# Kernel tuning notes

Measured on AMD Instinct MI355X. Metric: run time of the kernel, lower is better.

The kernel has to match this reference:

```python
import jax, jax.numpy as jnp
import numpy as np

RES_LIST = (16, 23, 32, 46, 64, 92, 128, 184, 256, 368, 512, 736)
NUM_DIM = 3
N_FEATURES = 2
LOG2_HASHMAP = 19
MAX_PARAMS = 2 ** LOG2_HASHMAP
N_POINTS = 2_000_000
PRIMES = (1, 2654435761, 805459861)  # Instant-NGP spatial hash primes


def _grid_meta():
    offsets, off = [], 0
    for r in RES_LIST:
        p = min(MAX_PARAMS, r ** NUM_DIM)
        p = int(np.ceil(p / 8) * 8)  # align to 8 as in __init__
        offsets.append(off)
        off += p
    offsets.append(off)
    return np.array(offsets, np.int32), off


def setup_inputs() -> dict:
    key = jax.random.key(0)
    k1, k2 = jax.random.split(key)
    offsets_np, total = _grid_meta()
    inputs = jax.random.uniform(k1, (N_POINTS, NUM_DIM), dtype=jnp.float32)
    std = 1e-4  # reset_parameters(): uniform(-1e-4, 1e-4)
    embeddings = jax.random.uniform(k2, (total, N_FEATURES), dtype=jnp.float32,
                                    minval=-std, maxval=std)
    return {
        "inputs": inputs,
        "embeddings": embeddings,
        "offsets_list": jnp.asarray(offsets_np),
        "resolutions_list": jnp.asarray(np.array(RES_LIST, np.int32)),
    }


def _encode(inputs, embeddings, offsets_list, resolutions_list):
    N = inputs.shape[0]
    F = embeddings.shape[1]
    params_in_level = (offsets_list[1:] - offsets_list[:-1]).astype(jnp.uint32)
    res = resolutions_list.astype(jnp.int32)
    # hash only when the dense grid does not fit in the hashmap
    use_hash = (res * res * res) > MAX_PARAMS  # res^3 < 2^31, safe in int32
    p0 = jnp.uint32(PRIMES[0]); p1 = jnp.uint32(PRIMES[1]); p2 = jnp.uint32(PRIMES[2])

    def level_fn(r, off, pil, uh):
        scale = (r - 1).astype(inputs.dtype)
        pos = inputs * scale                      # [N,3] in [0, res-1)
        f0 = jnp.floor(pos)
        w = pos - f0                              # trilinear fractions
        f0u = f0.astype(jnp.uint32)
        ru = r.astype(jnp.uint32)
        out = jnp.zeros((N, F), embeddings.dtype)
        for c in range(2 ** NUM_DIM):             # 8 corners (fixed small loop)
            bits = jnp.array([(c >> d) & 1 for d in range(NUM_DIM)], jnp.uint32)
            idx = f0u + bits                      # [N,3] corner grid coords
            wb = jnp.where(bits.astype(bool), w, 1.0 - w)
            weight = wb[:, 0] * wb[:, 1] * wb[:, 2]
            lin = idx[:, 0] + idx[:, 1] * ru + idx[:, 2] * ru * ru
            h = (idx[:, 0] * p0) ^ (idx[:, 1] * p1) ^ (idx[:, 2] * p2)
            flat = jnp.where(uh, h, lin) % pil    # uint32 wraparound hash
            g = embeddings[off + flat.astype(jnp.int32)]  # [N,F] gather
            out = out + weight[:, None] * g
        return out

    outs = jax.vmap(level_fn)(res, offsets_list[:-1], params_in_level, use_hash)
    # [L,N,F] -> [N, L*F], matching permute(1,0,2).reshape
    return outs.transpose(1, 0, 2).reshape(N, -1)


def reference(inputs, embeddings, offsets_list, resolutions_list):
    return _encode(inputs, embeddings, offsets_list, resolutions_list)
```

## Files before the change

kernel.cpp:

```cpp
#include <hip/hip_runtime.h>
#include <hip/hip_fp16.h>


namespace {
constexpr int NLEV = 12;
constexpr int BLOCK = 256;
constexpr int TOTAL = 4078528;
constexpr int DENSE_A_END = 146368;
constexpr int L4_SIZE = 262144;
constexpr unsigned P1 = 2654435761u;
constexpr unsigned P2 = 805459861u;
constexpr unsigned HMASK = (1u << 19) - 1u;

__device__ __constant__ constexpr int kRes[NLEV] = {
    16, 23, 32, 46, 64, 92, 128, 184, 256, 368, 512, 736};
__device__ __constant__ constexpr int kOff[NLEV] = {
    0, 4096, 16264, 49032, 146368, 408512,
    932800, 1457088, 1981376, 2505664, 3029952, 3554240};

typedef float    f32x2 __attribute__((ext_vector_type(2)));
typedef unsigned u32x2 __attribute__((ext_vector_type(2)));

__device__ __forceinline__ unsigned pkh2(float a, float b) {
    __half2 h = __floats2half2_rn(a, b);
    return *reinterpret_cast<unsigned*>(&h);
}
__device__ __forceinline__ float lo2f(unsigned u) {
    __half2 h = *reinterpret_cast<__half2*>(&u);
    return __low2float(h);
}
__device__ __forceinline__ float hi2f(unsigned u) {
    __half2 h = *reinterpret_cast<__half2*>(&u);
    return __high2float(h);
}
}

__global__ void __launch_bounds__(BLOCK)
pack_table_kernel(const float2* __restrict__ emb,
                  unsigned* __restrict__ packed, int total)
{
    int i = blockIdx.x * BLOCK + threadIdx.x;
    if (i < total) {
        float2 v = emb[i];
        packed[i] = pkh2(v.x, v.y);
    }
}

__global__ void __launch_bounds__(BLOCK)
pack_quad_kernel(const float2* __restrict__ emb, uint4* __restrict__ quad)
{
    int i = blockIdx.x * BLOCK + threadIdx.x;
    if (i >= DENSE_A_END) return;
    int R = (i < 4096) ? 16 : (i < 16264) ? 23 : (i < 49032) ? 32 : 46;
    float2 e0 = emb[i];
    float2 e1 = emb[i + 1];
    float2 e2 = emb[i + R];
    float2 e3 = emb[i + R + 1];
    uint4 q;
    q.x = pkh2(e0.x, e0.y); q.y = pkh2(e1.x, e1.y);
    q.z = pkh2(e2.x, e2.y); q.w = pkh2(e3.x, e3.y);
    quad[i] = q;
}

__global__ void __launch_bounds__(BLOCK)
pack_pair4_kernel(const float2* __restrict__ emb, u32x2* __restrict__ pair4)
{
    int i = blockIdx.x * BLOCK + threadIdx.x;
    if (i >= L4_SIZE) return;
    int g = DENSE_A_END + i;
    float2 a = emb[g];
    float2 b = emb[g + 1];
    u32x2 o;
    o.x = pkh2(a.x, a.y);
    o.y = pkh2(b.x, b.y);
    pair4[i] = o;
}

__global__ void __launch_bounds__(BLOCK)
dense_a_kernel(const float* __restrict__ inp, const uint4* __restrict__ quad,
               unsigned* __restrict__ stage, int N)
{
    const int tid = blockIdx.x * BLOCK + threadIdx.x;
    const int p0 = 2 * tid;
    if (p0 >= N) return;

    const f32x2* ip2 = reinterpret_cast<const f32x2*>(inp);
    const f32x2 v0 = ip2[3 * tid + 0];
    const f32x2 v1 = ip2[3 * tid + 1];
    const f32x2 v2 = ip2[3 * tid + 2];
    const float X[2] = {v0.x, v1.y};
    const float Y[2] = {v0.y, v2.x};
    const float Z[2] = {v1.x, v2.y};

#pragma unroll
    for (int l = 0; l < 4; ++l) {
        const unsigned R = (unsigned)kRes[l];
        const unsigned R2 = R * R;
        const float scale = (float)(kRes[l] - 1);
        const uint4* qt = quad + kOff[l];
        u32x2 res;
#pragma unroll
        for (int k = 0; k < 2; ++k) {
            const float px = X[k] * scale, py = Y[k] * scale, pz = Z[k] * scale;
            const float fx = floorf(px), fy = floorf(py), fz = floorf(pz);
            const float rx = px - fx, ry = py - fy, rz = pz - fz;
            const unsigned ix = (unsigned)fx, iy = (unsigned)fy,
                           iz = (unsigned)fz;
            const unsigned base = ix + iy * R + iz * R2;
            const uint4 q0 = qt[base];
            const uint4 q1 = qt[base + R2];
            const float wx0 = 1.0f - rx, wx1 = rx;
            const float wy0 = 1.0f - ry, wy1 = ry;
            const float wz0 = 1.0f - rz, wz1 = rz;
            const float ex00 = wx0 * lo2f(q0.x) + wx1 * lo2f(q0.y);
            const float ey00 = wx0 * hi2f(q0.x) + wx1 * hi2f(q0.y);
            const float ex10 = wx0 * lo2f(q0.z) + wx1 * lo2f(q0.w);
            const float ey10 = wx0 * hi2f(q0.z) + wx1 * hi2f(q0.w);
            const float ex01 = wx0 * lo2f(q1.x) + wx1 * lo2f(q1.y);
            const float ey01 = wx0 * hi2f(q1.x) + wx1 * hi2f(q1.y);
            const float ex11 = wx0 * lo2f(q1.z) + wx1 * lo2f(q1.w);
            const float ey11 = wx0 * hi2f(q1.z) + wx1 * hi2f(q1.w);
            const float sx = wz0 * (wy0 * ex00 + wy1 * ex10) +
                             wz1 * (wy0 * ex01 + wy1 * ex11);
            const float sy = wz0 * (wy0 * ey00 + wy1 * ey10) +
                             wz1 * (wy0 * ey01 + wy1 * ey11);
            res[k] = pkh2(sx, sy);
        }
        if (p0 + 1 < N) {
            __builtin_nontemporal_store(
                res, reinterpret_cast<u32x2*>(&stage[(long long)l * N + p0]));
        } else {
            __builtin_nontemporal_store(res.x, &stage[(long long)l * N + p0]);
        }
    }
}

__global__ void __launch_bounds__(BLOCK)
dense_b_kernel(const float* __restrict__ inp, const u32x2* __restrict__ pair4,
               unsigned* __restrict__ stage4, int N)
{
    const int tid = blockIdx.x * BLOCK + threadIdx.x;
    const int p0 = 2 * tid;
    if (p0 >= N) return;

    const f32x2* ip2 = reinterpret_cast<const f32x2*>(inp);
    const f32x2 v0 = ip2[3 * tid + 0];
    const f32x2 v1 = ip2[3 * tid + 1];
    const f32x2 v2 = ip2[3 * tid + 2];
    const float X[2] = {v0.x, v1.y};
    const float Y[2] = {v0.y, v2.x};
    const float Z[2] = {v1.x, v2.y};

    constexpr unsigned R = 64, R2 = 4096;
    constexpr float scale = 63.0f;
    u32x2 res;
#pragma unroll
    for (int k = 0; k < 2; ++k) {
        const float px = X[k] * scale, py = Y[k] * scale, pz = Z[k] * scale;
        const float fx = floorf(px), fy = floorf(py), fz = floorf(pz);
        const float rx = px - fx, ry = py - fy, rz = pz - fz;
        const unsigned ix = (unsigned)fx, iy = (unsigned)fy, iz = (unsigned)fz;
        const unsigned base = ix + iy * R + iz * R2;
        const u32x2 q00 = pair4[base];
        const u32x2 q10 = pair4[base + R];
        const u32x2 q01 = pair4[base + R2];
        const u32x2 q11 = pair4[base + R2 + R];
        const float wx0 = 1.0f - rx, wx1 = rx;
        const float wy0 = 1.0f - ry, wy1 = ry;
        const float wz0 = 1.0f - rz, wz1 = rz;
        const float w00 = wy0 * wz0, w10 = wy1 * wz0;
        const float w01 = wy0 * wz1, w11 = wy1 * wz1;
        float sx = 0.0f, sy = 0.0f;
        sx = fmaf(w00 * wx0, lo2f(q00.x), fmaf(w00 * wx1, lo2f(q00.y), sx));
        sy = fmaf(w00 * wx0, hi2f(q00.x), fmaf(w00 * wx1, hi2f(q00.y), sy));
        sx = fmaf(w10 * wx0, lo2f(q10.x), fmaf(w10 * wx1, lo2f(q10.y), sx));
        sy = fmaf(w10 * wx0, hi2f(q10.x), fmaf(w10 * wx1, hi2f(q10.y), sy));
        sx = fmaf(w01 * wx0, lo2f(q01.x), fmaf(w01 * wx1, lo2f(q01.y), sx));
        sy = fmaf(w01 * wx0, hi2f(q01.x), fmaf(w01 * wx1, hi2f(q01.y), sy));
        sx = fmaf(w11 * wx0, lo2f(q11.x), fmaf(w11 * wx1, lo2f(q11.y), sx));
        sy = fmaf(w11 * wx0, hi2f(q11.x), fmaf(w11 * wx1, hi2f(q11.y), sy));
        res[k] = pkh2(sx, sy);
    }
    if (p0 + 1 < N) {
        __builtin_nontemporal_store(res, reinterpret_cast<u32x2*>(&stage4[p0]));
    } else {
        __builtin_nontemporal_store(res.x, &stage4[p0]);
    }
}

template <int L>
__device__ __forceinline__ unsigned
encode_hash(float x, float y, float z, const unsigned* __restrict__ pt)
{
    const float scale = (float)(kRes[L] - 1);
    const float px = x * scale, py = y * scale, pz = z * scale;
    const float fx = floorf(px), fy = floorf(py), fz = floorf(pz);
    const float rx = px - fx, ry = py - fy, rz = pz - fz;
    const unsigned ix = (unsigned)fx, iy = (unsigned)fy, iz = (unsigned)fz;
    const unsigned yA = iy * P1, yB = yA + P1;
    const unsigned zA = iz * P2, zB = zA + P2;
    const unsigned h00 = (ix ^ yA ^ zA) & HMASK;
    const unsigned h10 = (ix ^ yB ^ zA) & HMASK;
    const unsigned h01 = (ix ^ yA ^ zB) & HMASK;
    const unsigned h11 = (ix ^ yB ^ zB) & HMASK;

    const u32x2* pt2 = reinterpret_cast<const u32x2*>(pt);
    const u32x2 q00 = pt2[h00 >> 1];
    const u32x2 q10 = pt2[h10 >> 1];
    const u32x2 q01 = pt2[h01 >> 1];
    const u32x2 q11 = pt2[h11 >> 1];

    unsigned e00 = (h00 & 1) ? q00.y : q00.x;
    unsigned e10 = (h10 & 1) ? q10.y : q10.x;
    unsigned e01 = (h01 & 1) ? q01.y : q01.x;
    unsigned e11 = (h11 & 1) ? q11.y : q11.x;
    unsigned f00 = (h00 & 1) ? q00.x : q00.y;
    unsigned f10 = (h10 & 1) ? q10.x : q10.y;
    unsigned f01 = (h01 & 1) ? q01.x : q01.y;
    unsigned f11 = (h11 & 1) ? q11.x : q11.y;

    if (ix & 1u) {
        const unsigned xo = ix + 1u;
        f00 = pt[(xo ^ yA ^ zA) & HMASK];
        f10 = pt[(xo ^ yB ^ zA) & HMASK];
        f01 = pt[(xo ^ yA ^ zB) & HMASK];
        f11 = pt[(xo ^ yB ^ zB) & HMASK];
    }

    const float wx0 = 1.0f - rx, wx1 = rx;
    const float wy0 = 1.0f - ry, wy1 = ry;
    const float wz0 = 1.0f - rz, wz1 = rz;
    const float w00 = wy0 * wz0, w10 = wy1 * wz0;
    const float w01 = wy0 * wz1, w11 = wy1 * wz1;
    float sx = 0.0f, sy = 0.0f;
    sx = fmaf(w00 * wx0, lo2f(e00), fmaf(w00 * wx1, lo2f(f00), sx));
    sy = fmaf(w00 * wx0, hi2f(e00), fmaf(w00 * wx1, hi2f(f00), sy));
    sx = fmaf(w10 * wx0, lo2f(e10), fmaf(w10 * wx1, lo2f(f10), sx));
    sy = fmaf(w10 * wx0, hi2f(e10), fmaf(w10 * wx1, hi2f(f10), sy));
    sx = fmaf(w01 * wx0, lo2f(e01), fmaf(w01 * wx1, lo2f(f01), sx));
    sy = fmaf(w01 * wx0, hi2f(e01), fmaf(w01 * wx1, hi2f(f01), sy));
    sx = fmaf(w11 * wx0, lo2f(e11), fmaf(w11 * wx1, lo2f(f11), sx));
    sy = fmaf(w11 * wx0, hi2f(e11), fmaf(w11 * wx1, hi2f(f11), sy));
    return pkh2(sx, sy);
}

template <int L>
__global__ void __launch_bounds__(BLOCK)
hash_kernel(const float* __restrict__ inp, const unsigned* __restrict__ packed,
            unsigned* __restrict__ stage_l, int N)
{
    const int tid = blockIdx.x * BLOCK + threadIdx.x;
    const int p0 = 2 * tid;
    if (p0 >= N) return;

    const f32x2* ip2 = reinterpret_cast<const f32x2*>(inp);
    const f32x2 v0 = ip2[3 * tid + 0];
    const f32x2 v1 = ip2[3 * tid + 1];
    const f32x2 v2 = ip2[3 * tid + 2];

    const unsigned* pt = packed + kOff[L];
    u32x2 res;
    res.x = encode_hash<L>(v0.x, v0.y, v1.x, pt);
    res.y = encode_hash<L>(v1.y, v2.x, v2.y, pt);

    if (p0 + 1 < N) {
        __builtin_nontemporal_store(res, reinterpret_cast<u32x2*>(&stage_l[p0]));
    } else {
        __builtin_nontemporal_store(res.x, &stage_l[p0]);
    }
}

__global__ void __launch_bounds__(BLOCK)
assemble_kernel(const unsigned* __restrict__ lvl, float* __restrict__ out,
                int N)
{
    __shared__ float s_out[BLOCK * 25];
    const int t = threadIdx.x;
    const int n = blockIdx.x * BLOCK + t;

    if (n < N) {
#pragma unroll
        for (int l = 0; l < NLEV; ++l) {
            unsigned u = __builtin_nontemporal_load(&lvl[(long long)l * N + n]);
            s_out[t * 25 + 2 * l + 0] = lo2f(u);
            s_out[t * 25 + 2 * l + 1] = hi2f(u);
        }
    }
    __syncthreads();

    const long long base = (long long)blockIdx.x * (BLOCK * 24);
    const long long lim = (long long)N * 24;
#pragma unroll
    for (int k = 0; k < 24; ++k) {
        const int g = k * BLOCK + t;
        const long long gg = base + g;
        if (gg < lim) {
            const int nl = g / 24;
            const int j = g - nl * 24;
            __builtin_nontemporal_store(s_out[nl * 25 + j], &out[gg]);
        }
    }
}

template <int PACKED>
__global__ void __launch_bounds__(BLOCK, 4)
fused_kernel(const float* __restrict__ inp, const void* __restrict__ table,
             float* __restrict__ out, int N)
{
    __shared__ float s_out[BLOCK * 25];
    const int t = threadIdx.x;
    const int n = blockIdx.x * BLOCK + t;

    if (n < N) {
        const float x = inp[n * 3 + 0];
        const float y = inp[n * 3 + 1];
        const float z = inp[n * 3 + 2];

#pragma unroll
        for (int l = 0; l < NLEV; ++l) {
            const int R = kRes[l];
            const bool HASH = (l >= 5);
            const float scale = (float)(R - 1);
            const float px = x * scale, py = y * scale, pz = z * scale;
            const float fx = floorf(px), fy = floorf(py), fz = floorf(pz);
            const float wx = px - fx, wy = py - fy, wz = pz - fz;
            const unsigned ix = (unsigned)fx, iy = (unsigned)fy,
                           iz = (unsigned)fz;
            unsigned x0, x1, y0, y1, z0, z1;
            if (HASH) {
                x0 = ix;      x1 = ix + 1u;
                y0 = iy * P1; y1 = y0 + P1;
                z0 = iz * P2; z1 = z0 + P2;
            } else {
                const unsigned Ru = (unsigned)R, R2 = Ru * Ru;
                x0 = ix;      x1 = ix + 1u;
                y0 = iy * Ru; y1 = y0 + Ru;
                z0 = iz * R2; z1 = z0 + R2;
            }
            unsigned idx[8];
            if (HASH) {
                idx[0] = (x0 ^ y0 ^ z0) & HMASK; idx[1] = (x1 ^ y0 ^ z0) & HMASK;
                idx[2] = (x0 ^ y1 ^ z0) & HMASK; idx[3] = (x1 ^ y1 ^ z0) & HMASK;
                idx[4] = (x0 ^ y0 ^ z1) & HMASK; idx[5] = (x1 ^ y0 ^ z1) & HMASK;
                idx[6] = (x0 ^ y1 ^ z1) & HMASK; idx[7] = (x1 ^ y1 ^ z1) & HMASK;
            } else {
                idx[0] = x0 + y0 + z0; idx[1] = x1 + y0 + z0;
                idx[2] = x0 + y1 + z0; idx[3] = x1 + y1 + z0;
                idx[4] = x0 + y0 + z1; idx[5] = x1 + y0 + z1;
                idx[6] = x0 + y1 + z1; idx[7] = x1 + y1 + z1;
            }
            float ex[8], ey[8];
            if (PACKED) {
                const unsigned* eb =
                    reinterpret_cast<const unsigned*>(table) + kOff[l];
#pragma unroll
                for (int c = 0; c < 8; ++c) {
                    unsigned uu = eb[idx[c]];
                    ex[c] = lo2f(uu); ey[c] = hi2f(uu);
                }
            } else {
                const float2* eb =
                    reinterpret_cast<const float2*>(table) + kOff[l];
#pragma unroll
                for (int c = 0; c < 8; ++c) {
                    float2 e = eb[idx[c]]; ex[c] = e.x; ey[c] = e.y;
                }
            }
            const float w0x = 1.0f - wx, w0y = 1.0f - wy, w0z = 1.0f - wz;
            const float w00 = w0x * w0y, w10 = wx * w0y;
            const float w01 = w0x * wy,  w11 = wx * wy;
            const float wt[8] = {w00 * w0z, w10 * w0z, w01 * w0z, w11 * w0z,
                                 w00 * wz,  w10 * wz,  w01 * wz,  w11 * wz};
            float sx = 0.0f, sy = 0.0f;
#pragma unroll
            for (int c = 0; c < 8; ++c) {
                sx = fmaf(wt[c], ex[c], sx);
                sy = fmaf(wt[c], ey[c], sy);
            }
            s_out[t * 25 + 2 * l + 0] = sx;
            s_out[t * 25 + 2 * l + 1] = sy;
        }
    }
    __syncthreads();
    const long long base = (long long)blockIdx.x * (BLOCK * 24);
    const long long lim = (long long)N * 24;
#pragma unroll
    for (int k = 0; k < 24; ++k) {
        const int g = k * BLOCK + t;
        const long long gg = base + g;
        if (gg < lim) {
            const int nl = g / 24;
            const int j = g - nl * 24;
            out[gg] = s_out[nl * 25 + j];
        }
    }
}

extern "C" void kernel_launch(void* const* d_in, const int* in_sizes, int n_in,
                              void* d_out, int out_size, void* d_ws, size_t ws_size,
                              hipStream_t stream) {
    const float* inputs = (const float*)d_in[0];
    const float* embeddings = (const float*)d_in[1];
    float* out = (float*)d_out;

    const int N = in_sizes[0] / 3;
    const int total = in_sizes[1] / 2;

    const size_t quad_bytes = (size_t)DENSE_A_END * 16;
    const size_t pair4_bytes = (size_t)L4_SIZE * 8;
    const size_t packed_bytes = (size_t)total * sizeof(unsigned);
    const size_t stage_bytes = (size_t)NLEV * N * sizeof(unsigned);

    const int ngrid = (N + BLOCK - 1) / BLOCK;
    const int grid2 = (N / 2 + BLOCK - 1) / BLOCK;

    if (ws_size >= quad_bytes + pair4_bytes + packed_bytes + stage_bytes) {
        char* w = (char*)d_ws;
        uint4* quad = (uint4*)w;                  w += quad_bytes;
        u32x2* pair4 = (u32x2*)w;                 w += pair4_bytes;
        unsigned* packed = (unsigned*)w;          w += packed_bytes;
        unsigned* stage = (unsigned*)w;

        pack_table_kernel<<<(total + BLOCK - 1) / BLOCK, BLOCK, 0, stream>>>(
            (const float2*)embeddings, packed, total);
        pack_quad_kernel<<<(DENSE_A_END + BLOCK - 1) / BLOCK, BLOCK, 0, stream>>>(
            (const float2*)embeddings, quad);
        pack_pair4_kernel<<<(L4_SIZE + BLOCK - 1) / BLOCK, BLOCK, 0, stream>>>(
            (const float2*)embeddings, pair4);

        dense_a_kernel<<<grid2, BLOCK, 0, stream>>>(inputs, quad, stage, N);
        dense_b_kernel<<<grid2, BLOCK, 0, stream>>>(inputs, pair4,
                                                    stage + 4LL * N, N);
        hash_kernel<5><<<grid2, BLOCK, 0, stream>>>(inputs, packed, stage + 5LL * N, N);
        hash_kernel<6><<<grid2, BLOCK, 0, stream>>>(inputs, packed, stage + 6LL * N, N);
        hash_kernel<7><<<grid2, BLOCK, 0, stream>>>(inputs, packed, stage + 7LL * N, N);
        hash_kernel<8><<<grid2, BLOCK, 0, stream>>>(inputs, packed, stage + 8LL * N, N);
        hash_kernel<9><<<grid2, BLOCK, 0, stream>>>(inputs, packed, stage + 9LL * N, N);
        hash_kernel<10><<<grid2, BLOCK, 0, stream>>>(inputs, packed, stage + 10LL * N, N);
        hash_kernel<11><<<grid2, BLOCK, 0, stream>>>(inputs, packed, stage + 11LL * N, N);
        assemble_kernel<<<ngrid, BLOCK, 0, stream>>>(stage, out, N);
    } else if (ws_size >= packed_bytes) {
        unsigned* packed = (unsigned*)d_ws;
        pack_table_kernel<<<(total + BLOCK - 1) / BLOCK, BLOCK, 0, stream>>>(
            (const float2*)embeddings, packed, total);
        fused_kernel<1><<<ngrid, BLOCK, 0, stream>>>(inputs, packed, out, N);
    } else {
        fused_kernel<0><<<ngrid, BLOCK, 0, stream>>>(inputs, embeddings, out, N);
    }
}
```

Measured before the change: 530.2 us.

## Merge pack kernels and fuse per-level encode kernels into one launch

Combines the three embedding-packing kernels into one pack kernel that reads each embedding once for the flat table and reuses it for the quad and pair layouts. Replaces the nine per-level encode launches (dense A, dense B, seven hash levels) with one kernel whose block index selects the level group, so all levels can run concurrently across the GPU. This targets launch overhead and the tail idle time between small dependent launches. In exchange the hash level becomes a runtime value rather than a template parameter, and the middle fallback path no longer uses the packed table.

After: 490.3 us. 7.5% less time.

```diff
diff --git a/kernel.cpp b/kernel.cpp
--- a/kernel.cpp
+++ b/kernel.cpp
@@ -36,163 +36,38 @@
 }
 
 __global__ void __launch_bounds__(BLOCK)
-pack_table_kernel(const float2* __restrict__ emb,
-                  unsigned* __restrict__ packed, int total)
+pack_all_kernel(const float2* __restrict__ emb,
+                unsigned* __restrict__ packed,
+                uint4* __restrict__ quad,
+                u32x2* __restrict__ pair4, int total)
 {
     int i = blockIdx.x * BLOCK + threadIdx.x;
-    if (i < total) {
-        float2 v = emb[i];
-        packed[i] = pkh2(v.x, v.y);
-    }
-}
-
-__global__ void __launch_bounds__(BLOCK)
-pack_quad_kernel(const float2* __restrict__ emb, uint4* __restrict__ quad)
+    if (i >= total) return;
+    float2 v = emb[i];
+    packed[i] = pkh2(v.x, v.y);
+    if (i < DENSE_A_END) {
+        int R = (i < 4096) ? 16 : (i < 16264) ? 23 : (i < 49032) ? 32 : 46;
+        float2 e1 = emb[i + 1];
+        float2 e2 = emb[i + R];
+        float2 e3 = emb[i + R + 1];
+        uint4 q;
+        q.x = pkh2(v.x, v.y);  q.y = pkh2(e1.x, e1.y);
+        q.z = pkh2(e2.x, e2.y); q.w = pkh2(e3.x, e3.y);
+        quad[i] = q;
+    }
+    if (i < L4_SIZE) {
+        int g = DENSE_A_END + i;
+        float2 a = emb[g];
+        float2 b = emb[g + 1];
+        u32x2 o; o.x = pkh2(a.x, a.y); o.y = pkh2(b.x, b.y);
+        pair4[i] = o;
+    }
+}
+
+__device__ __forceinline__ unsigned
+encode_hash_rt(float x, float y, float z, const unsigned* __restrict__ pt,
+               float scale)
 {
-    int i = blockIdx.x * BLOCK + threadIdx.x;
-    if (i >= DENSE_A_END) return;
-    int R = (i < 4096) ? 16 : (i < 16264) ? 23 : (i < 49032) ? 32 : 46;
-    float2 e0 = emb[i];
-    float2 e1 = emb[i + 1];
-    float2 e2 = emb[i + R];
-    float2 e3 = emb[i + R + 1];
-    uint4 q;
-    q.x = pkh2(e0.x, e0.y); q.y = pkh2(e1.x, e1.y);
-    q.z = pkh2(e2.x, e2.y); q.w = pkh2(e3.x, e3.y);
-    quad[i] = q;
-}
-
-__global__ void __launch_bounds__(BLOCK)
-pack_pair4_kernel(const float2* __restrict__ emb, u32x2* __restrict__ pair4)
-{
-    int i = blockIdx.x * BLOCK + threadIdx.x;
-    if (i >= L4_SIZE) return;
-    int g = DENSE_A_END + i;
-    float2 a = emb[g];
-    float2 b = emb[g + 1];
-    u32x2 o;
-    o.x = pkh2(a.x, a.y);
-    o.y = pkh2(b.x, b.y);
-    pair4[i] = o;
-}
-
-__global__ void __launch_bounds__(BLOCK)
-dense_a_kernel(const float* __restrict__ inp, const uint4* __restrict__ quad,
-               unsigned* __restrict__ stage, int N)
-{
-    const int tid = blockIdx.x * BLOCK + threadIdx.x;
-    const int p0 = 2 * tid;
-    if (p0 >= N) return;
-
-    const f32x2* ip2 = reinterpret_cast<const f32x2*>(inp);
-    const f32x2 v0 = ip2[3 * tid + 0];
-    const f32x2 v1 = ip2[3 * tid + 1];
-    const f32x2 v2 = ip2[3 * tid + 2];
-    const float X[2] = {v0.x, v1.y};
-    const float Y[2] = {v0.y, v2.x};
-    const float Z[2] = {v1.x, v2.y};
-
-#pragma unroll
-    for (int l = 0; l < 4; ++l) {
-        const unsigned R = (unsigned)kRes[l];
-        const unsigned R2 = R * R;
-        const float scale = (float)(kRes[l] - 1);
-        const uint4* qt = quad + kOff[l];
-        u32x2 res;
-#pragma unroll
-        for (int k = 0; k < 2; ++k) {
-            const float px = X[k] * scale, py = Y[k] * scale, pz = Z[k] * scale;
-            const float fx = floorf(px), fy = floorf(py), fz = floorf(pz);
-            const float rx = px - fx, ry = py - fy, rz = pz - fz;
-            const unsigned ix = (unsigned)fx, iy = (unsigned)fy,
-                           iz = (unsigned)fz;
-            const unsigned base = ix + iy * R + iz * R2;
-            const uint4 q0 = qt[base];
-            const uint4 q1 = qt[base + R2];
-            const float wx0 = 1.0f - rx, wx1 = rx;
-            const float wy0 = 1.0f - ry, wy1 = ry;
-            const float wz0 = 1.0f - rz, wz1 = rz;
-            const float ex00 = wx0 * lo2f(q0.x) + wx1 * lo2f(q0.y);
-            const float ey00 = wx0 * hi2f(q0.x) + wx1 * hi2f(q0.y);
-            const float ex10 = wx0 * lo2f(q0.z) + wx1 * lo2f(q0.w);
-            const float ey10 = wx0 * hi2f(q0.z) + wx1 * hi2f(q0.w);
-            const float ex01 = wx0 * lo2f(q1.x) + wx1 * lo2f(q1.y);
-            const float ey01 = wx0 * hi2f(q1.x) + wx1 * hi2f(q1.y);
-            const float ex11 = wx0 * lo2f(q1.z) + wx1 * lo2f(q1.w);
-            const float ey11 = wx0 * hi2f(q1.z) + wx1 * hi2f(q1.w);
-            const float sx = wz0 * (wy0 * ex00 + wy1 * ex10) +
-                             wz1 * (wy0 * ex01 + wy1 * ex11);
-            const float sy = wz0 * (wy0 * ey00 + wy1 * ey10) +
-                             wz1 * (wy0 * ey01 + wy1 * ey11);
-            res[k] = pkh2(sx, sy);
-        }
-        if (p0 + 1 < N) {
-            __builtin_nontemporal_store(
-                res, reinterpret_cast<u32x2*>(&stage[(long long)l * N + p0]));
-        } else {
-            __builtin_nontemporal_store(res.x, &stage[(long long)l * N + p0]);
-        }
-    }
-}
-
-__global__ void __launch_bounds__(BLOCK)
-dense_b_kernel(const float* __restrict__ inp, const u32x2* __restrict__ pair4,
-               unsigned* __restrict__ stage4, int N)
-{
-    const int tid = blockIdx.x * BLOCK + threadIdx.x;
-    const int p0 = 2 * tid;
-    if (p0 >= N) return;
-
-    const f32x2* ip2 = reinterpret_cast<const f32x2*>(inp);
-    const f32x2 v0 = ip2[3 * tid + 0];
-    const f32x2 v1 = ip2[3 * tid + 1];
-    const f32x2 v2 = ip2[3 * tid + 2];
-    const float X[2] = {v0.x, v1.y};
-    const float Y[2] = {v0.y, v2.x};
-    const float Z[2] = {v1.x, v2.y};
-
-    constexpr unsigned R = 64, R2 = 4096;
-    constexpr float scale = 63.0f;
-    u32x2 res;
-#pragma unroll
-    for (int k = 0; k < 2; ++k) {
-        const float px = X[k] * scale, py = Y[k] * scale, pz = Z[k] * scale;
-        const float fx = floorf(px), fy = floorf(py), fz = floorf(pz);
-        const float rx = px - fx, ry = py - fy, rz = pz - fz;
-        const unsigned ix = (unsigned)fx, iy = (unsigned)fy, iz = (unsigned)fz;
-        const unsigned base = ix + iy * R + iz * R2;
-        const u32x2 q00 = pair4[base];
-        const u32x2 q10 = pair4[base + R];
-        const u32x2 q01 = pair4[base + R2];
-        const u32x2 q11 = pair4[base + R2 + R];
-        const float wx0 = 1.0f - rx, wx1 = rx;
-        const float wy0 = 1.0f - ry, wy1 = ry;
-        const float wz0 = 1.0f - rz, wz1 = rz;
-        const float w00 = wy0 * wz0, w10 = wy1 * wz0;
-        const float w01 = wy0 * wz1, w11 = wy1 * wz1;
-        float sx = 0.0f, sy = 0.0f;
-        sx = fmaf(w00 * wx0, lo2f(q00.x), fmaf(w00 * wx1, lo2f(q00.y), sx));
-        sy = fmaf(w00 * wx0, hi2f(q00.x), fmaf(w00 * wx1, hi2f(q00.y), sy));
-        sx = fmaf(w10 * wx0, lo2f(q10.x), fmaf(w10 * wx1, lo2f(q10.y), sx));
-        sy = fmaf(w10 * wx0, hi2f(q10.x), fmaf(w10 * wx1, hi2f(q10.y), sy));
-        sx = fmaf(w01 * wx0, lo2f(q01.x), fmaf(w01 * wx1, lo2f(q01.y), sx));
-        sy = fmaf(w01 * wx0, hi2f(q01.x), fmaf(w01 * wx1, hi2f(q01.y), sy));
-        sx = fmaf(w11 * wx0, lo2f(q11.x), fmaf(w11 * wx1, lo2f(q11.y), sx));
-        sy = fmaf(w11 * wx0, hi2f(q11.x), fmaf(w11 * wx1, hi2f(q11.y), sy));
-        res[k] = pkh2(sx, sy);
-    }
-    if (p0 + 1 < N) {
-        __builtin_nontemporal_store(res, reinterpret_cast<u32x2*>(&stage4[p0]));
-    } else {
-        __builtin_nontemporal_store(res.x, &stage4[p0]);
-    }
-}
-
-template <int L>
-__device__ __forceinline__ unsigned
-encode_hash(float x, float y, float z, const unsigned* __restrict__ pt)
-{
-    const float scale = (float)(kRes[L] - 1);
     const float px = x * scale, py = y * scale, pz = z * scale;
     const float fx = floorf(px), fy = floorf(py), fz = floorf(pz);
     const float rx = px - fx, ry = py - fy, rz = pz - fz;
@@ -244,29 +119,128 @@
     return pkh2(sx, sy);
 }
 
-template <int L>
 __global__ void __launch_bounds__(BLOCK)
-hash_kernel(const float* __restrict__ inp, const unsigned* __restrict__ packed,
-            unsigned* __restrict__ stage_l, int N)
+mega_kernel(const float* __restrict__ inp,
+            const uint4* __restrict__ quad,
+            const u32x2* __restrict__ pair4,
+            const unsigned* __restrict__ packed,
+            unsigned* __restrict__ stage, int N, int CB)
 {
-    const int tid = blockIdx.x * BLOCK + threadIdx.x;
-    const int p0 = 2 * tid;
+    const int b = blockIdx.x;
+    const int t = b / CB;
+    const int chunk = b - t * CB;
+    const int g = chunk * BLOCK + threadIdx.x;
+    const int p0 = 2 * g;
     if (p0 >= N) return;
+    const bool two = (p0 + 1 < N);
 
     const f32x2* ip2 = reinterpret_cast<const f32x2*>(inp);
-    const f32x2 v0 = ip2[3 * tid + 0];
-    const f32x2 v1 = ip2[3 * tid + 1];
-    const f32x2 v2 = ip2[3 * tid + 2];
-
-    const unsigned* pt = packed + kOff[L];
-    u32x2 res;
-    res.x = encode_hash<L>(v0.x, v0.y, v1.x, pt);
-    res.y = encode_hash<L>(v1.y, v2.x, v2.y, pt);
-
-    if (p0 + 1 < N) {
-        __builtin_nontemporal_store(res, reinterpret_cast<u32x2*>(&stage_l[p0]));
+    f32x2 v0 = ip2[3 * g + 0];
+    f32x2 v1, v2;
+    if (two) { v1 = ip2[3 * g + 1]; v2 = ip2[3 * g + 2]; }
+    else { v1.x = inp[3 * p0 + 2]; v1.y = 0.0f; v2.x = 0.0f; v2.y = 0.0f; }
+    const float X[2] = {v0.x, v1.y};
+    const float Y[2] = {v0.y, v2.x};
+    const float Z[2] = {v1.x, v2.y};
+
+    if (t == 0) {
+#pragma unroll
+        for (int l = 0; l < 4; ++l) {
+            const unsigned R = (unsigned)kRes[l];
+            const unsigned R2 = R * R;
+            const float scale = (float)(kRes[l] - 1);
+            const uint4* qt = quad + kOff[l];
+            u32x2 res;
+#pragma unroll
+            for (int k = 0; k < 2; ++k) {
+                const float px = X[k] * scale, py = Y[k] * scale,
+                            pz = Z[k] * scale;
+                const float fx = floorf(px), fy = floorf(py), fz = floorf(pz);
+                const float rx = px - fx, ry = py - fy, rz = pz - fz;
+                const unsigned ix = (unsigned)fx, iy = (unsigned)fy,
+                               iz = (unsigned)fz;
+                const unsigned base = ix + iy * R + iz * R2;
+                const uint4 q0 = qt[base];
+                const uint4 q1 = qt[base + R2];
+                const float wx0 = 1.0f - rx, wx1 = rx;
+                const float wy0 = 1.0f - ry, wy1 = ry;
+                const float wz0 = 1.0f - rz, wz1 = rz;
+                const float ex00 = wx0 * lo2f(q0.x) + wx1 * lo2f(q0.y);
+                const float ey00 = wx0 * hi2f(q0.x) + wx1 * hi2f(q0.y);
+                const float ex10 = wx0 * lo2f(q0.z) + wx1 * lo2f(q0.w);
+                const float ey10 = wx0 * hi2f(q0.z) + wx1 * hi2f(q0.w);
+                const float ex01 = wx0 * lo2f(q1.x) + wx1 * lo2f(q1.y);
+                const float ey01 = wx0 * hi2f(q1.x) + wx1 * hi2f(q1.y);
+                const float ex11 = wx0 * lo2f(q1.z) + wx1 * lo2f(q1.w);
+                const float ey11 = wx0 * hi2f(q1.z) + wx1 * hi2f(q1.w);
+                const float sx = wz0 * (wy0 * ex00 + wy1 * ex10) +
+                                 wz1 * (wy0 * ex01 + wy1 * ex11);
+                const float sy = wz0 * (wy0 * ey00 + wy1 * ey10) +
+                                 wz1 * (wy0 * ey01 + wy1 * ey11);
+                res[k] = pkh2(sx, sy);
+            }
+            if (two) {
+                __builtin_nontemporal_store(
+                    res,
+                    reinterpret_cast<u32x2*>(&stage[(long long)l * N + p0]));
+            } else {
+                __builtin_nontemporal_store(res.x,
+                                            &stage[(long long)l * N + p0]);
+            }
+        }
+    } else if (t == 1) {
+        constexpr unsigned R = 64, R2 = 4096;
+        constexpr float scale = 63.0f;
+        u32x2 res;
+#pragma unroll
+        for (int k = 0; k < 2; ++k) {
+            const float px = X[k] * scale, py = Y[k] * scale, pz = Z[k] * scale;
+            const float fx = floorf(px), fy = floorf(py), fz = floorf(pz);
+            const float rx = px - fx, ry = py - fy, rz = pz - fz;
+            const unsigned ix = (unsigned)fx, iy = (unsigned)fy,
+                           iz = (unsigned)fz;
+            const unsigned base = ix + iy * R + iz * R2;
+            const u32x2 q00 = pair4[base];
+            const u32x2 q10 = pair4[base + R];
+            const u32x2 q01 = pair4[base + R2];
+            const u32x2 q11 = pair4[base + R2 + R];
+            const float wx0 = 1.0f - rx, wx1 = rx;
+            const float wy0 = 1.0f - ry, wy1 = ry;
+            const float wz0 = 1.0f - rz, wz1 = rz;
+            const float w00 = wy0 * wz0, w10 = wy1 * wz0;
+            const float w01 = wy0 * wz1, w11 = wy1 * wz1;
+            float sx = 0.0f, sy = 0.0f;
+            sx = fmaf(w00 * wx0, lo2f(q00.x), fmaf(w00 * wx1, lo2f(q00.y), sx));
+            sy = fmaf(w00 * wx0, hi2f(q00.x), fmaf(w00 * wx1, hi2f(q00.y), sy));
+            sx = fmaf(w10 * wx0, lo2f(q10.x), fmaf(w10 * wx1, lo2f(q10.y), sx));
+            sy = fmaf(w10 * wx0, hi2f(q10.x), fmaf(w10 * wx1, hi2f(q10.y), sy));
+            sx = fmaf(w01 * wx0, lo2f(q01.x), fmaf(w01 * wx1, lo2f(q01.y), sx));
+            sy = fmaf(w01 * wx0, hi2f(q01.x), fmaf(w01 * wx1, hi2f(q01.y), sy));
+            sx = fmaf(w11 * wx0, lo2f(q11.x), fmaf(w11 * wx1, lo2f(q11.y), sx));
+            sy = fmaf(w11 * wx0, hi2f(q11.x), fmaf(w11 * wx1, hi2f(q11.y), sy));
+            res[k] = pkh2(sx, sy);
+        }
+        unsigned* s4 = stage + 4LL * N;
+        if (two) {
+            __builtin_nontemporal_store(res,
+                                        reinterpret_cast<u32x2*>(&s4[p0]));
+        } else {
+            __builtin_nontemporal_store(res.x, &s4[p0]);
+        }
     } else {
-        __builtin_nontemporal_store(res.x, &stage_l[p0]);
+        const int L = t + 3;
+        const float scale = (float)(kRes[L] - 1);
+        const unsigned* pt = packed + kOff[L];
+        u32x2 res;
+        res.x = encode_hash_rt(X[0], Y[0], Z[0], pt, scale);
+        res.y = two ? encode_hash_rt(X[1], Y[1], Z[1], pt, scale) : 0u;
+        unsigned* sl = stage + (long long)L * N;
+        if (two) {
+            __builtin_nontemporal_store(res,
+                                        reinterpret_cast<u32x2*>(&sl[p0]));
+        } else {
+            __builtin_nontemporal_store(res.x, &sl[p0]);
+        }
     }
 }
 
@@ -412,7 +386,6 @@
     const size_t stage_bytes = (size_t)NLEV * N * sizeof(unsigned);
 
     const int ngrid = (N + BLOCK - 1) / BLOCK;
-    const int grid2 = (N / 2 + BLOCK - 1) / BLOCK;
 
     if (ws_size >= quad_bytes + pair4_bytes + packed_bytes + stage_bytes) {
         char* w = (char*)d_ws;
@@ -421,29 +394,18 @@
         unsigned* packed = (unsigned*)w;          w += packed_bytes;
         unsigned* stage = (unsigned*)w;
 
-        pack_table_kernel<<<(total + BLOCK - 1) / BLOCK, BLOCK, 0, stream>>>(
-            (const float2*)embeddings, packed, total);
-        pack_quad_kernel<<<(DENSE_A_END + BLOCK - 1) / BLOCK, BLOCK, 0, stream>>>(
-            (const float2*)embeddings, quad);
-        pack_pair4_kernel<<<(L4_SIZE + BLOCK - 1) / BLOCK, BLOCK, 0, stream>>>(
-            (const float2*)embeddings, pair4);
-
-        dense_a_kernel<<<grid2, BLOCK, 0, stream>>>(inputs, quad, stage, N);
-        dense_b_kernel<<<grid2, BLOCK, 0, stream>>>(inputs, pair4,
-                                                    stage + 4LL * N, N);
-        hash_kernel<5><<<grid2, BLOCK, 0, stream>>>(inputs, packed, stage + 5LL * N, N);
-        hash_kernel<6><<<grid2, BLOCK, 0, stream>>>(inputs, packed, stage + 6LL * N, N);
-        hash_kernel<7><<<grid2, BLOCK, 0, stream>>>(inputs, packed, stage + 7LL * N, N);
-        hash_kernel<8><<<grid2, BLOCK, 0, stream>>>(inputs, packed, stage + 8LL * N, N);
-        hash_kernel<9><<<grid2, BLOCK, 0, stream>>>(inputs, packed, stage + 9LL * N, N);
-        hash_kernel<10><<<grid2, BLOCK, 0, stream>>>(inputs, packed, stage + 10LL * N, N);
-        hash_kernel<11><<<grid2, BLOCK, 0, stream>>>(inputs, packed, stage + 11LL * N, N);
+        pack_all_kernel<<<(total + BLOCK - 1) / BLOCK, BLOCK, 0, stream>>>(
+            (const float2*)embeddings, packed, quad, pair4, total);
+
+        const int pairs = (N + 1) / 2;
+        const int CB = (pairs + BLOCK - 1) / BLOCK;
+        mega_kernel<<<9 * CB, BLOCK, 0, stream>>>(
+            inputs, quad, pair4, packed, stage, N, CB);
+
         assemble_kernel<<<ngrid, BLOCK, 0, stream>>>(stage, out, N);
     } else if (ws_size >= packed_bytes) {
         unsigned* packed = (unsigned*)d_ws;
-        pack_table_kernel<<<(total + BLOCK - 1) / BLOCK, BLOCK, 0, stream>>>(
-            (const float2*)embeddings, packed, total);
-        fused_kernel<1><<<ngrid, BLOCK, 0, stream>>>(inputs, packed, out, N);
+        fused_kernel<0><<<ngrid, BLOCK, 0, stream>>>(inputs, embeddings, out, N);
     } else {
         fused_kernel<0><<<ngrid, BLOCK, 0, stream>>>(inputs, embeddings, out, N);
     }
```
